# Kernel tuning notes

Measured on AMD Instinct MI355X. Metric: run time of the kernel, lower is better.

Reference implementation:

```python
import jax, jax.numpy as jnp
import numpy as np

B, S, VOCAB, HID, NCLS = 64, 512, 1400, 256, 128


def _time_lstm(W_all, b_all, U_all, b_u, W_d, b_d, x, ts):
    # x: [b, s, h], ts: [b, s]
    b = x.shape[0]
    h0 = jnp.zeros((b, HID), x.dtype)
    c0 = jnp.zeros((b, HID), x.dtype)

    def step(carry, xt):
        h, c = carry
        x_t, t_t = xt  # [b,h], [b]
        c_s1 = jnp.tanh(c @ W_d.T + b_d)
        c_adj = (c - c_s1) + c_s1 * t_t[:, None]
        gates = jax.nn.sigmoid(h @ W_all.T + b_all + x_t @ U_all.T + b_u)
        f, i, o, c_tmp = jnp.split(gates, 4, axis=1)  # note: c_tmp is sigmoid, as in source
        c_new = f * c_adj + i * c_tmp
        h_new = o * jnp.tanh(c_new)
        return (h_new, c_new), h_new

    _, hs = jax.lax.scan(step, (h0, c0), (x.transpose(1, 0, 2), ts.T))
    return hs.transpose(1, 0, 2)  # [b, s, h]


def setup_inputs() -> dict:
    key = jax.random.key(0)
    ks = jax.random.split(key, 18)

    def g(k, shape, scale=0.05):
        return jax.random.normal(k, shape, dtype=jnp.float32) * scale

    return {
        "inputs": jax.random.uniform(ks[0], (B, S, VOCAB), dtype=jnp.float32),
        "timestamps": jax.random.uniform(ks[1], (B, S), dtype=jnp.float32),
        "emb": g(ks[2], (VOCAB, HID)),
        "W_all1": g(ks[3], (4 * HID, HID)), "b_all1": g(ks[4], (4 * HID,)),
        "U_all1": g(ks[5], (4 * HID, HID)), "b_u1": g(ks[6], (4 * HID,)),
        "W_d1": g(ks[7], (HID, HID)), "b_d1": g(ks[8], (HID,)),
        "W_all2": g(ks[9], (4 * HID, HID)), "b_all2": g(ks[10], (4 * HID,)),
        "U_all2": g(ks[11], (4 * HID, HID)), "b_u2": g(ks[12], (4 * HID,)),
        "W_d2": g(ks[13], (HID, HID)), "b_d2": g(ks[14], (HID,)),
        "wa": g(ks[15], (1, HID)),
        "Wb": g(ks[16], (HID, HID)),
        "W_out": g(ks[17], (NCLS, HID)),
    }


def reference(inputs, timestamps, emb, W_all1, b_all1, U_all1, b_u1, W_d1, b_d1,
              W_all2, b_all2, U_all2, b_u2, W_d2, b_d2, wa, Wb, W_out):
    embedded = jnp.einsum('bsv,vh->bsh', inputs, emb)  # multi-hot embedding lookup
    out1 = _time_lstm(W_all1, b_all1, U_all1, b_u1, W_d1, b_d1, embedded, timestamps)
    out2 = _time_lstm(W_all2, b_all2, U_all2, b_u2, W_d2, b_d2, embedded, timestamps)
    alpha = jax.nn.softmax(jnp.einsum('bsh,oh->bs', out1, wa), axis=1)  # [b,s]
    Beta = jnp.tanh(jnp.einsum('bsh,gh->bsg', out2, Wb))  # [b,s,h]
    ctx = jnp.sum(embedded * Beta * alpha[:, :, None], axis=1)  # [b,h]
    return ctx @ W_out.T  # [b, num_classes]
```

## Files before the change

kernel.cpp:

```cpp
#include <hip/hip_runtime.h>

typedef __attribute__((ext_vector_type(8))) short short8;
typedef __attribute__((ext_vector_type(4))) float f32x4;
typedef __attribute__((ext_vector_type(4))) unsigned int u32x4;

#define B_   64
#define S_   512
#define V_   1400
#define VP_  1408
#define H_   256
#define G4_  1024
#define NC_  128
#define CH_  64

__device__ __forceinline__ unsigned short f2bf(float f) {
    unsigned u = __builtin_bit_cast(unsigned, f);
    u += 0x7FFFu + ((u >> 16) & 1u);
    return (unsigned short)(u >> 16);
}
__device__ __forceinline__ float bf2f(unsigned short h) {
    unsigned u = ((unsigned)h) << 16;
    return __builtin_bit_cast(float, u);
}
__device__ __forceinline__ float fsig(float x) {
    x = fminf(fmaxf(x, -40.f), 40.f);
    float e = __builtin_amdgcn_exp2f(x * -1.44269504f);
    return __builtin_amdgcn_rcpf(1.0f + e);
}
__device__ __forceinline__ float ftanh(float x) {
    x = fminf(fmaxf(x, -40.f), 40.f);
    float e = __builtin_amdgcn_exp2f(x * 2.88539008f);
    return 1.0f - 2.0f * __builtin_amdgcn_rcpf(e + 1.0f);
}

__device__ __forceinline__ short8 gload16_sc1(const unsigned short* p) {
    short8 r;
    asm volatile("global_load_dwordx4 %0, %1, off sc1"
                 : "=&v"(r) : "v"((unsigned long long)p));
    return r;
}
__device__ __forceinline__ void gstore_short_sc1(unsigned short* p, unsigned v) {
    asm volatile("global_store_short %0, %1, off sc1"
                 :: "v"((unsigned long long)p), "v"(v));
}
__device__ __forceinline__ short8 gload16_sc0(const unsigned short* p) {
    short8 r;
    asm volatile("global_load_dwordx4 %0, %1, off sc0"
                 : "=&v"(r) : "v"((unsigned long long)p));
    return r;
}
__device__ __forceinline__ void gstore_short_plain(unsigned short* p, unsigned v) {
    asm volatile("global_store_short %0, %1, off"
                 :: "v"((unsigned long long)p), "v"(v));
}
__device__ __forceinline__ void gstore_dword_plain(unsigned int* p, unsigned v) {
    asm volatile("global_store_dword %0, %1, off"
                 :: "v"((unsigned long long)p), "v"(v));
}
__device__ __forceinline__ void gpoll16_plain(const unsigned int* p,
                                              u32x4& f0, u32x4& f1, u32x4& f2, u32x4& f3) {
    asm volatile("global_load_dwordx4 %0, %4, off\n\t"
                 "global_load_dwordx4 %1, %5, off\n\t"
                 "global_load_dwordx4 %2, %6, off\n\t"
                 "global_load_dwordx4 %3, %7, off\n\t"
                 "s_waitcnt vmcnt(0)"
                 : "=&v"(f0), "=&v"(f1), "=&v"(f2), "=&v"(f3)
                 : "v"((unsigned long long)p),        "v"((unsigned long long)(p + 4)),
                   "v"((unsigned long long)(p + 8)),  "v"((unsigned long long)(p + 12)));
}

#define CNT_ZONE_ 38912

__global__ void k0_prep(const float* __restrict__ emb,
                        const float* __restrict__ Wa1, const float* __restrict__ Wa2,
                        const float* __restrict__ Wd1, const float* __restrict__ Wd2,
                        const float* __restrict__ U1,  const float* __restrict__ U2,
                        const float* __restrict__ ba1, const float* __restrict__ bu1,
                        const float* __restrict__ ba2, const float* __restrict__ bu2,
                        const float* __restrict__ Wb,
                        unsigned short* __restrict__ embT, unsigned short* __restrict__ Wg,
                        unsigned short* __restrict__ Wd,   unsigned short* __restrict__ Ub,
                        unsigned short* __restrict__ Wbb,  float* __restrict__ bg,
                        unsigned int* __restrict__ cnt) {
    int tid = blockIdx.x * blockDim.x + threadIdx.x;
    int np = gridDim.x * blockDim.x;
    for (int i = tid; i < 256 * VP_; i += np) {
        int n = i / VP_, k = i - n * VP_;
        embT[i] = (k < V_) ? f2bf(emb[k * H_ + n]) : (unsigned short)0;
    }
    for (int i = tid; i < G4_ * H_; i += np) {
        Wg[i] = f2bf(Wa1[i]); Wg[G4_ * H_ + i] = f2bf(Wa2[i]);
        Ub[i] = f2bf(U1[i]);  Ub[G4_ * H_ + i] = f2bf(U2[i]);
    }
    for (int i = tid; i < H_ * H_; i += np) {
        Wd[i] = f2bf(Wd1[i]); Wd[H_ * H_ + i] = f2bf(Wd2[i]); Wbb[i] = f2bf(Wb[i]);
    }
    for (int i = tid; i < G4_; i += np) {
        bg[i] = ba1[i] + bu1[i]; bg[G4_ + i] = ba2[i] + bu2[i];
    }
    for (int i = tid; i < CNT_ZONE_; i += np) cnt[i] = 0;
}

__global__ __launch_bounds__(512, 2) void k1_embed(const float* __restrict__ inputs,
                                                   const unsigned short* __restrict__ embT,
                                                   unsigned short* __restrict__ embB) {
    const int tid = threadIdx.x;
    const int w = tid >> 6, ln = tid & 63, q = ln >> 4, l16 = ln & 15;
    const int mt = w >> 2, ng = (w & 3) * 4;
    const int Rbase = blockIdx.x * 32 + mt * 16;
    const float* arow = inputs + (long)(Rbase + l16) * V_;

    f32x4 acc[4];
    #pragma unroll
    for (int i = 0; i < 4; ++i) acc[i] = (f32x4){0.f, 0.f, 0.f, 0.f};

    for (int kt = 0; kt < 44; ++kt) {
        int k0 = kt * 32 + q * 8;
        short8 af;
        if (kt == 43 && q == 3) {
            #pragma unroll
            for (int j = 0; j < 8; ++j) af[j] = 0;
        } else {
            f32x4 x0 = *(const f32x4*)(arow + k0);
            f32x4 x1 = *(const f32x4*)(arow + k0 + 4);
            #pragma unroll
            for (int j = 0; j < 4; ++j) { af[j] = (short)f2bf(x0[j]); af[4 + j] = (short)f2bf(x1[j]); }
        }
        #pragma unroll
        for (int i = 0; i < 4; ++i) {
            short8 bf = *(const short8*)(embT + (long)((ng + i) * 16 + l16) * VP_ + k0);
            acc[i] = __builtin_amdgcn_mfma_f32_16x16x32_bf16(af, bf, acc[i], 0, 0, 0);
        }
    }
    #pragma unroll
    for (int i = 0; i < 4; ++i) {
        int col = (ng + i) * 16 + l16;
        #pragma unroll
        for (int j = 0; j < 4; ++j) {
            int R = Rbase + 4 * q + j;
            embB[(long)R * H_ + col] = f2bf(acc[i][j]);
        }
    }
}

__global__ __launch_bounds__(512, 2) void k2_pre(const unsigned short* __restrict__ embB,
                                                 const unsigned short* __restrict__ Ub,
                                                 const float* __restrict__ bg,
                                                 float* __restrict__ P, int t0) {
    const int tid = threadIdx.x;
    const int w = tid >> 6, ln = tid & 63, q = ln >> 4, l16 = ln & 15;
    const int rbase = blockIdx.x * 32;

    short8 af[2][8];
    #pragma unroll
    for (int mt = 0; mt < 2; ++mt)
        #pragma unroll
        for (int kt = 0; kt < 8; ++kt) {
            int rp = rbase + mt * 16 + l16;
            int rg = t0 * 64 + rp;
            int b = rg & 63, s = rg >> 6;
            af[mt][kt] = *(const short8*)(embB + ((long)b * S_ + s) * H_ + kt * 32 + q * 8);
        }

    for (int i = 0; i < 16; ++i) {
        int nt2 = w * 16 + i;
        int l = nt2 >> 6;
        int gcol = (nt2 & 63) * 16 + l16;
        float bias = bg[nt2 * 16 + l16];
        short8 bf[8];
        #pragma unroll
        for (int kt = 0; kt < 8; ++kt)
            bf[kt] = *(const short8*)(Ub + (long)(nt2 * 16 + l16) * H_ + kt * 32 + q * 8);
        #pragma unroll
        for (int mt = 0; mt < 2; ++mt) {
            f32x4 acc = (f32x4){bias, bias, bias, bias};
            #pragma unroll
            for (int kt = 0; kt < 8; ++kt)
                acc = __builtin_amdgcn_mfma_f32_16x16x32_bf16(af[mt][kt], bf[kt], acc, 0, 0, 0);
            int rp0 = rbase + mt * 16;
            float* dst = P + ((long)l * (CH_ * 64) + rp0 + 4 * q) * G4_ + gcol;
            #pragma unroll
            for (int j = 0; j < 4; ++j) dst[(long)j * G4_] = acc[j];
        }
    }
}

__global__ __launch_bounds__(256, 1) void k3_fused(const float* __restrict__ ts,
                                                   const unsigned short* __restrict__ W,
                                                   const float* __restrict__ bd1,
                                                   const float* __restrict__ bd2,
                                                   const float* __restrict__ Pcur,
                                                   unsigned short* __restrict__ out1,
                                                   unsigned short* __restrict__ out2,
                                                   float* __restrict__ cst,
                                                   unsigned short* __restrict__ cx,
                                                   unsigned int* __restrict__ cnt,
                                                   int t0,
                                                   const unsigned short* __restrict__ embB,
                                                   const unsigned short* __restrict__ Ub,
                                                   const float* __restrict__ bg,
                                                   float* __restrict__ Pnext,
                                                   int next_t0) {
    const int tid = threadIdx.x;
    const int w = tid >> 6, ln = tid & 63, q = ln >> 4, l16 = ln & 15;
    const int bid = blockIdx.x;

    if (bid >= 32) {
        const int g2 = bid - 32;
        const int rbase = (g2 >> 1) * 32;
        const int hb = g2 & 1;

        short8 af[2][8];
        #pragma unroll
        for (int mt = 0; mt < 2; ++mt)
            #pragma unroll
            for (int kt = 0; kt < 8; ++kt) {
                int rp = rbase + mt * 16 + l16;
                int rg = next_t0 * 64 + rp;
                int b = rg & 63, s = rg >> 6;
                af[mt][kt] = *(const short8*)(embB + ((long)b * S_ + s) * H_ + kt * 32 + q * 8);
            }

        for (int i = 0; i < 16; ++i) {
            int nt2 = hb * 64 + w * 16 + i;
            int l = nt2 >> 6;
            int gcol = (nt2 & 63) * 16 + l16;
            float bias = bg[nt2 * 16 + l16];
            short8 bf[8];
            #pragma unroll
            for (int kt = 0; kt < 8; ++kt)
                bf[kt] = *(const short8*)(Ub + (long)(nt2 * 16 + l16) * H_ + kt * 32 + q * 8);
            #pragma unroll
            for (int mt = 0; mt < 2; ++mt) {
                f32x4 acc = (f32x4){bias, bias, bias, bias};
                #pragma unroll
                for (int kt = 0; kt < 8; ++kt)
                    acc = __builtin_amdgcn_mfma_f32_16x16x32_bf16(af[mt][kt], bf[kt], acc, 0, 0, 0);
                int rp0 = rbase + mt * 16;
                float* dst = Pnext + ((long)l * (CH_ * 64) + rp0 + 4 * q) * G4_ + gcol;
                #pragma unroll
                for (int j = 0; j < 4; ++j) dst[(long)j * G4_] = acc[j];
            }
        }
        return;
    }

    __shared__ float ts_lds[16][CH_];
    const int chunk = t0 >> 6;

    const int myx = (int)__builtin_amdgcn_s_getreg(63508);
    unsigned int* rdy  = cnt + 4096 + chunk * 64;
    int*          xpub = (int*)(cnt + 4608);
    if (tid == 0) {
        __hip_atomic_store(&xpub[bid], myx, __ATOMIC_RELAXED, __HIP_MEMORY_SCOPE_AGENT);
        __hip_atomic_fetch_add(rdy, 1u, __ATOMIC_RELEASE, __HIP_MEMORY_SCOPE_AGENT);
    }
    unsigned hs_it = 0;
    while (__hip_atomic_load(rdy, __ATOMIC_ACQUIRE, __HIP_MEMORY_SCOPE_AGENT) < 32u
           && ++hs_it < (1u << 20))
        __builtin_amdgcn_s_sleep(2);
    int xv[32];
    #pragma unroll
    for (int i = 0; i < 32; ++i)
        xv[i] = __hip_atomic_load(&xpub[i], __ATOMIC_RELAXED, __HIP_MEMORY_SCOPE_AGENT);
    unsigned okA = 1, inr = 1, mask = 0;
    #pragma unroll
    for (int g = 0; g < 8; ++g)
        okA &= (unsigned)((xv[g] == xv[g + 8]) & (xv[g] == xv[g + 16]) & (xv[g] == xv[g + 24]));
    #pragma unroll
    for (int i = 0; i < 32; ++i) {
        inr &= (unsigned)((unsigned)xv[i] < 8u);
        mask |= 1u << ((unsigned)xv[i] & 31u);
    }
    const bool fast = okA && inr && (mask == 0xFFu) && (hs_it < (1u << 20));

    const int grp = bid & 7, cg = bid >> 3;
    const int l = grp >> 2, m = grp & 3, b0 = m * 16;
    const int hc0 = cg * 64 + w * 16;
    const int mycol = hc0 + l16;
    unsigned int* cell = cnt + (chunk * 8 + grp) * 64;
    unsigned int* fbase = cnt + 6144 + (long)chunk * 64 * 64;
    unsigned short* outp = l ? out2 : out1;
    const float bdv = (l ? bd2 : bd1)[mycol];

    for (int i = tid; i < 16 * CH_; i += 256) {
        int r = i >> 6, cc = i & (CH_ - 1);
        ts_lds[r][cc] = ts[(b0 + r) * S_ + t0 + cc];
    }

    short8 wg[4][8];
    short8 wd[8];
    #pragma unroll
    for (int g = 0; g < 4; ++g)
        #pragma unroll
        for (int kt = 0; kt < 8; ++kt)
            wg[g][kt] = *(const short8*)(W + ((long)(l * G4_ + g * H_ + mycol)) * H_ + kt * 32 + q * 8);
    #pragma unroll
    for (int kt = 0; kt < 8; ++kt)
        wd[kt] = *(const short8*)(W + (long)2 * G4_ * H_ + ((long)(l * H_ + mycol)) * H_ + kt * 32 + q * 8);

    float cf[4];
    if (t0 == 0) {
        cf[0] = cf[1] = cf[2] = cf[3] = 0.f;
    } else {
        #pragma unroll
        for (int j = 0; j < 4; ++j)
            cf[j] = cst[(long)(l * 4 + m) * 4096 + (4 * q + j) * 256 + mycol];
    }
    __syncthreads();

    const float* Pbase = Pcur + ((long)l * (CH_ * 64) + b0) * G4_;

    if (fast) {
        unsigned opaque_zero;
        asm volatile("v_mov_b32 %0, 0" : "=v"(opaque_zero));

        float pv[4][4];
        #pragma unroll
        for (int g = 0; g < 4; ++g)
            #pragma unroll
            for (int j = 0; j < 4; ++j)
                pv[g][j] = Pbase[((long)(4 * q + j)) * G4_ + g * H_ + mycol];
        asm volatile("" ::: "memory");

        #pragma unroll 1
        for (int t = 0; t < CH_; ++t) {
            const int gt = t0 + t;

            if (t) {
                const unsigned int* fprev = fbase + (long)(t - 1) * 64;
                u32x4 f0, f1, f2, f3;
                gpoll16_plain(fprev, f0, f1, f2, f3);
                unsigned s = 0;
                #pragma unroll
                for (int i = 0; i < 4; ++i) s += f0[i] + f1[i] + f2[i] + f3[i];
                if (s != 16u) {
                    const unsigned tgt = 16u * (unsigned)t;
                    unsigned it = 0;
                    for (;;) {
                        unsigned v = 0;
                        if (ln == 0)
                            v = __hip_atomic_fetch_add(cell, opaque_zero,
                                                       __ATOMIC_RELAXED, __HIP_MEMORY_SCOPE_WORKGROUP);
                        v = __shfl(v, 0);
                        if (v >= tgt || ++it >= (1u << 14)) break;
                    }
                }
            }
            __builtin_amdgcn_fence(__ATOMIC_ACQUIRE, "agent");
            __builtin_amdgcn_sched_barrier(0);

            short8 ha[8], ca[8];
            if (gt == 0) {
                #pragma unroll
                for (int kt = 0; kt < 8; ++kt) {
                    #pragma unroll
                    for (int j = 0; j < 8; ++j) { ha[kt][j] = 0; ca[kt][j] = 0; }
                }
            } else {
                const unsigned short* crow = cx + ((long)(((gt - 1) & 1) * 8 + grp)) * 4096 + l16 * 256 + q * 8;
                const unsigned short* hrow = outp + ((long)(b0 + l16) * S_ + (gt - 1)) * H_ + q * 8;
                #pragma unroll
                for (int kt = 0; kt < 8; ++kt) ca[kt] = gload16_sc0(crow + kt * 32);
                #pragma unroll
                for (int kt = 0; kt < 8; ++kt) ha[kt] = gload16_sc0(hrow + kt * 32);
            }
            asm volatile("s_waitcnt vmcnt(8)" ::: "memory");
            __builtin_amdgcn_sched_barrier(0);

            f32x4 dacc = (f32x4){bdv, bdv, bdv, bdv};
            #pragma unroll
            for (int kt = 0; kt < 8; ++kt)
                dacc = __builtin_amdgcn_mfma_f32_16x16x32_bf16(ca[kt], wd[kt], dacc, 0, 0, 0);

            asm volatile("s_waitcnt vmcnt(0)" ::: "memory");
            __builtin_amdgcn_sched_barrier(0);

            f32x4 gacc[4];
            #pragma unroll
            for (int g = 0; g < 4; ++g) {
                gacc[g] = (f32x4){pv[g][0], pv[g][1], pv[g][2], pv[g][3]};
                #pragma unroll
                for (int kt = 0; kt < 8; ++kt)
                    gacc[g] = __builtin_amdgcn_mfma_f32_16x16x32_bf16(ha[kt], wg[g][kt], gacc[g], 0, 0, 0);
            }

            #pragma unroll
            for (int j = 0; j < 4; ++j) {
                int r = 4 * q + j;
                float tv = ts_lds[r][t];
                float cs1 = ftanh(dacc[j]);
                float cadj = cf[j] + cs1 * (tv - 1.0f);
                float fg = fsig(gacc[0][j]), ig = fsig(gacc[1][j]);
                float og = fsig(gacc[2][j]), ct = fsig(gacc[3][j]);
                float cn = fg * cadj + ig * ct;
                float hn = og * ftanh(cn);
                cf[j] = cn;
                gstore_short_plain(outp + ((long)(b0 + r) * S_ + gt) * H_ + mycol, (unsigned)f2bf(hn));
                gstore_short_plain(cx + ((long)((gt & 1) * 8 + grp)) * 4096 + r * 256 + mycol, (unsigned)f2bf(cn));
            }
            asm volatile("s_waitcnt vmcnt(0)" ::: "memory");
            if (ln == 0) {
                gstore_dword_plain(fbase + (long)t * 64 + (cg * 4 + w), 1u);
                (void)__hip_atomic_fetch_add(cell, 1u, __ATOMIC_RELAXED, __HIP_MEMORY_SCOPE_WORKGROUP);
            }

            {
                int tn = (t + 1 < CH_) ? t + 1 : t;
                asm volatile("" ::: "memory");
                #pragma unroll
                for (int g = 0; g < 4; ++g)
                    #pragma unroll
                    for (int j = 0; j < 4; ++j)
                        pv[g][j] = Pbase[((long)tn * 64 + 4 * q + j) * G4_ + g * H_ + mycol];
                asm volatile("" ::: "memory");
            }
        }
    } else {
        #pragma unroll 1
        for (int t = 0; t < CH_; ++t) {
            const int gt = t0 + t;

            float pv[4][4];
            #pragma unroll
            for (int g = 0; g < 4; ++g)
                #pragma unroll
                for (int j = 0; j < 4; ++j)
                    pv[g][j] = Pbase[((long)t * 64 + 4 * q + j) * G4_ + g * H_ + mycol];
            asm volatile("" ::: "memory");

            {
                unsigned tgt = 4u * (unsigned)t, it = 0;
                while (__hip_atomic_load(cell, __ATOMIC_RELAXED, __HIP_MEMORY_SCOPE_AGENT) < tgt
                       && ++it < (1u << 18))
                    __builtin_amdgcn_s_sleep(1);
            }

            short8 ha[8], ca[8];
            if (gt == 0) {
                #pragma unroll
                for (int kt = 0; kt < 8; ++kt) {
                    #pragma unroll
                    for (int j = 0; j < 8; ++j) { ha[kt][j] = 0; ca[kt][j] = 0; }
                }
            } else {
                const unsigned short* crow = cx + ((long)(((gt - 1) & 1) * 8 + grp)) * 4096 + l16 * 256 + q * 8;
                const unsigned short* hrow = outp + ((long)(b0 + l16) * S_ + (gt - 1)) * H_ + q * 8;
                #pragma unroll
                for (int kt = 0; kt < 8; ++kt) ca[kt] = gload16_sc1(crow + kt * 32);
                #pragma unroll
                for (int kt = 0; kt < 8; ++kt) ha[kt] = gload16_sc1(hrow + kt * 32);
            }
            asm volatile("s_waitcnt vmcnt(8)" ::: "memory");
            __builtin_amdgcn_sched_barrier(0);

            f32x4 dacc = (f32x4){bdv, bdv, bdv, bdv};
            #pragma unroll
            for (int kt = 0; kt < 8; ++kt)
                dacc = __builtin_amdgcn_mfma_f32_16x16x32_bf16(ca[kt], wd[kt], dacc, 0, 0, 0);

            asm volatile("s_waitcnt vmcnt(0)" ::: "memory");
            __builtin_amdgcn_sched_barrier(0);

            f32x4 gacc[4];
            #pragma unroll
            for (int g = 0; g < 4; ++g) {
                gacc[g] = (f32x4){pv[g][0], pv[g][1], pv[g][2], pv[g][3]};
                #pragma unroll
                for (int kt = 0; kt < 8; ++kt)
                    gacc[g] = __builtin_amdgcn_mfma_f32_16x16x32_bf16(ha[kt], wg[g][kt], gacc[g], 0, 0, 0);
            }

            #pragma unroll
            for (int j = 0; j < 4; ++j) {
                int r = 4 * q + j;
                float tv = ts_lds[r][t];
                float cs1 = ftanh(dacc[j]);
                float cadj = cf[j] + cs1 * (tv - 1.0f);
                float fg = fsig(gacc[0][j]), ig = fsig(gacc[1][j]);
                float og = fsig(gacc[2][j]), ct = fsig(gacc[3][j]);
                float cn = fg * cadj + ig * ct;
                float hn = og * ftanh(cn);
                cf[j] = cn;
                gstore_short_sc1(outp + ((long)(b0 + r) * S_ + gt) * H_ + mycol, (unsigned)f2bf(hn));
                gstore_short_sc1(cx + ((long)((gt & 1) * 8 + grp)) * 4096 + r * 256 + mycol, (unsigned)f2bf(cn));
            }
            asm volatile("s_waitcnt vmcnt(0)" ::: "memory");
            __syncthreads();
            if (tid == 0) atomicAdd(cell, 1u);
        }
    }

    #pragma unroll
    for (int j = 0; j < 4; ++j)
        cst[(long)(l * 4 + m) * 4096 + (4 * q + j) * 256 + mycol] = cf[j];
}

__global__ __launch_bounds__(512) void k4a_alpha(const unsigned short* __restrict__ out1,
                                                 const float* __restrict__ wa,
                                                 float* __restrict__ alpha) {
    __shared__ float sc[512];
    __shared__ float red[512];
    const int b = blockIdx.x, tid = threadIdx.x;
    const int w = tid >> 6, ln = tid & 63;
    f32x4 wv = *(const f32x4*)(wa + ln * 4);
    for (int i = 0; i < 64; ++i) {
        int s = w * 64 + i;
        const unsigned short* row = out1 + ((long)b * S_ + s) * H_ + ln * 4;
        float d = bf2f(row[0]) * wv[0] + bf2f(row[1]) * wv[1] +
                  bf2f(row[2]) * wv[2] + bf2f(row[3]) * wv[3];
        #pragma unroll
        for (int off = 32; off; off >>= 1) d += __shfl_xor(d, off);
        if (ln == 0) sc[s] = d;
    }
    __syncthreads();
    float v = sc[tid];
    red[tid] = v;
    for (int st = 256; st; st >>= 1) {
        __syncthreads();
        if (tid < st) red[tid] = fmaxf(red[tid], red[tid + st]);
    }
    __syncthreads();
    float M = red[0];
    __syncthreads();
    float e = __builtin_amdgcn_exp2f((v - M) * 1.44269504f);
    red[tid] = e;
    for (int st = 256; st; st >>= 1) {
        __syncthreads();
        if (tid < st) red[tid] += red[tid + st];
    }
    __syncthreads();
    alpha[b * S_ + tid] = e * __builtin_amdgcn_rcpf(red[0]);
}

__global__ __launch_bounds__(512, 2) void k4b_ctx(const unsigned short* __restrict__ out2,
                                                  const unsigned short* __restrict__ Wbb,
                                                  const unsigned short* __restrict__ embB,
                                                  const float* __restrict__ alpha,
                                                  float* __restrict__ ctx) {
    __shared__ float cbuf[32][256];
    const int b = blockIdx.x, tid = threadIdx.x;
    const int w = tid >> 6, ln = tid & 63, q = ln >> 4, l16 = ln & 15;

    float cp[16];
    #pragma unroll
    for (int nt = 0; nt < 16; ++nt) cp[nt] = 0.f;

    for (int i = 0; i < 4; ++i) {
        int mt = w * 4 + i;
        short8 af[8];
        #pragma unroll
        for (int kt = 0; kt < 8; ++kt)
            af[kt] = *(const short8*)(out2 + ((long)b * S_ + mt * 16 + l16) * H_ + kt * 32 + q * 8);
        float al[4];
        #pragma unroll
        for (int j = 0; j < 4; ++j) al[j] = alpha[b * S_ + mt * 16 + 4 * q + j];
        for (int nt = 0; nt < 16; ++nt) {
            f32x4 acc = (f32x4){0.f, 0.f, 0.f, 0.f};
            #pragma unroll
            for (int kt = 0; kt < 8; ++kt) {
                short8 bf = *(const short8*)(Wbb + (long)(nt * 16 + l16) * H_ + kt * 32 + q * 8);
                acc = __builtin_amdgcn_mfma_f32_16x16x32_bf16(af[kt], bf, acc, 0, 0, 0);
            }
            #pragma unroll
            for (int j = 0; j < 4; ++j) {
                int s = mt * 16 + 4 * q + j;
                float beta = ftanh(acc[j]);
                float ev = bf2f(embB[((long)b * S_ + s) * H_ + nt * 16 + l16]);
                cp[nt] += beta * al[j] * ev;
            }
        }
    }
    #pragma unroll
    for (int nt = 0; nt < 16; ++nt) cbuf[w * 4 + q][nt * 16 + l16] = cp[nt];
    __syncthreads();
    if (tid < 256) {
        float sum = 0.f;
        for (int i = 0; i < 32; ++i) sum += cbuf[i][tid];
        ctx[b * H_ + tid] = sum;
    }
}

__global__ void k4c_out(const float* __restrict__ ctx, const float* __restrict__ Wout,
                        float* __restrict__ out) {
    int b = blockIdx.x, n = threadIdx.x;
    const f32x4* cr = (const f32x4*)(ctx + b * H_);
    const f32x4* wr = (const f32x4*)(Wout + n * H_);
    float acc = 0.f;
    #pragma unroll 8
    for (int i = 0; i < 64; ++i) {
        f32x4 c = cr[i], ww = wr[i];
        acc += c[0] * ww[0] + c[1] * ww[1] + c[2] * ww[2] + c[3] * ww[3];
    }
    out[b * NC_ + n] = acc;
}

extern "C" void kernel_launch(void* const* d_in, const int* in_sizes, int n_in,
                              void* d_out, int out_size, void* d_ws, size_t ws_size,
                              hipStream_t stream) {
    (void)in_sizes; (void)n_in; (void)out_size;
    const float* inputs = (const float*)d_in[0];
    const float* tsp    = (const float*)d_in[1];
    const float* emb    = (const float*)d_in[2];
    const float* Wa1 = (const float*)d_in[3];  const float* ba1 = (const float*)d_in[4];
    const float* U1  = (const float*)d_in[5];  const float* bu1 = (const float*)d_in[6];
    const float* Wd1 = (const float*)d_in[7];  const float* bd1 = (const float*)d_in[8];
    const float* Wa2 = (const float*)d_in[9];  const float* ba2 = (const float*)d_in[10];
    const float* U2  = (const float*)d_in[11]; const float* bu2 = (const float*)d_in[12];
    const float* Wd2 = (const float*)d_in[13]; const float* bd2 = (const float*)d_in[14];
    const float* wa  = (const float*)d_in[15];
    const float* Wb  = (const float*)d_in[16];
    const float* Wout = (const float*)d_in[17];
    float* out = (float*)d_out;

    char* ws = (char*)d_ws;
    unsigned short* embT = (unsigned short*)(ws + 0);
    unsigned short* Wg   = (unsigned short*)(ws + 720896);
    unsigned short* Wd   = (unsigned short*)(ws + 1769472);
    unsigned short* Ub   = (unsigned short*)(ws + 2031616);
    unsigned short* Wbb  = (unsigned short*)(ws + 3080192);
    float*          bgp  = (float*)(ws + 3211264);
    unsigned short* embB = (unsigned short*)(ws + 3219456);
    float*          P0   = (float*)(ws + 19996672);
    unsigned short* out1 = (unsigned short*)(ws + 53551104);
    unsigned short* out2 = (unsigned short*)(ws + 70328320);
    unsigned short* cx   = (unsigned short*)(ws + 87105536);
    float*          cst  = (float*)(ws + 87236608);
    float*          alp  = (float*)(ws + 87367680);
    float*          ctx  = (float*)(ws + 87498752);
    unsigned int*   cnt  = (unsigned int*)(ws + 87564288);
    float*          P1   = (float*)(ws + 87719936);
    const size_t NEED_FUSED = 121274368;
    const bool fuse = (ws_size >= NEED_FUSED);

    hipLaunchKernelGGL(k0_prep, dim3(256), dim3(256), 0, stream,
                       emb, Wa1, Wa2, Wd1, Wd2, U1, U2, ba1, bu1, ba2, bu2, Wb,
                       embT, Wg, Wd, Ub, Wbb, bgp, cnt);
    hipLaunchKernelGGL(k1_embed, dim3(1024), dim3(512), 0, stream, inputs, embT, embB);
    hipLaunchKernelGGL(k2_pre, dim3(128), dim3(512), 0, stream, embB, Ub, bgp, P0, 0);

    float* Pb[2] = { P0, fuse ? P1 : P0 };
    for (int c = 0; c < 8; ++c) {
        if (fuse) {
            int ng = (c < 7) ? 256 : 0;
            hipLaunchKernelGGL(k3_fused, dim3(32 + ng), dim3(256), 0, stream,
                               tsp, Wg, bd1, bd2, Pb[c & 1], out1, out2, cst, cx, cnt, c * CH_,
                               embB, Ub, bgp, Pb[(c + 1) & 1], (c + 1) * CH_);
        } else {
            if (c > 0)
                hipLaunchKernelGGL(k2_pre, dim3(128), dim3(512), 0, stream, embB, Ub, bgp, P0, c * CH_);
            hipLaunchKernelGGL(k3_fused, dim3(32), dim3(256), 0, stream,
                               tsp, Wg, bd1, bd2, P0, out1, out2, cst, cx, cnt, c * CH_,
                               embB, Ub, bgp, P0, S_ );
        }
    }
    hipLaunchKernelGGL(k4a_alpha, dim3(64), dim3(512), 0, stream, out1, wa, alp);
    hipLaunchKernelGGL(k4b_ctx, dim3(64), dim3(512), 0, stream, out2, Wbb, embB, alp, ctx);
    hipLaunchKernelGGL(k4c_out, dim3(64), dim3(128), 0, stream, ctx, Wout, out);
}
```

Measured before the change: 2.822 ms.

## Use per-group monotonic step flags and prefetch next projections before gate MFMAs

Per-timestep one-shot flags are replaced by one reusable flag slot per wave per group that stores a monotonically increasing step count. Consumers now spin on a 16-flag poll with an acquire fence each iteration and only fall back to the atomic counter after many retries. The prefetch of the next step's input projections also moves earlier, ahead of the gate MFMAs, so it overlaps compute rather than the flag publish. The aim is lower inter-block synchronisation latency in the recurrent loop, at the cost of repeated acquire fences in the spin loop and a changed flag memory layout.

```diff
diff --git a/kernel.cpp b/kernel.cpp
--- a/kernel.cpp
+++ b/kernel.cpp
@@ -279,7 +279,7 @@
     const int hc0 = cg * 64 + w * 16;
     const int mycol = hc0 + l16;
     unsigned int* cell = cnt + (chunk * 8 + grp) * 64;
-    unsigned int* fbase = cnt + 6144 + (long)chunk * 64 * 64;
+    unsigned int* fl   = cnt + 6144 + (chunk * 8 + grp) * 64;
     unsigned short* outp = l ? out2 : out1;
     const float bdv = (l ? bd2 : bd1)[mycol];
 
@@ -328,26 +328,36 @@
             const int gt = t0 + t;
 
             if (t) {
-                const unsigned int* fprev = fbase + (long)(t - 1) * 64;
-                u32x4 f0, f1, f2, f3;
-                gpoll16_plain(fprev, f0, f1, f2, f3);
-                unsigned s = 0;
-                #pragma unroll
-                for (int i = 0; i < 4; ++i) s += f0[i] + f1[i] + f2[i] + f3[i];
-                if (s != 16u) {
-                    const unsigned tgt = 16u * (unsigned)t;
-                    unsigned it = 0;
-                    for (;;) {
-                        unsigned v = 0;
-                        if (ln == 0)
-                            v = __hip_atomic_fetch_add(cell, opaque_zero,
-                                                       __ATOMIC_RELAXED, __HIP_MEMORY_SCOPE_WORKGROUP);
-                        v = __shfl(v, 0);
-                        if (v >= tgt || ++it >= (1u << 14)) break;
+                const unsigned tt = (unsigned)t;
+                unsigned it = 0;
+                for (;;) {
+                    __builtin_amdgcn_fence(__ATOMIC_ACQUIRE, "agent");
+                    u32x4 f0, f1, f2, f3;
+                    gpoll16_plain(fl, f0, f1, f2, f3);
+                    unsigned ok = 1;
+                    #pragma unroll
+                    for (int i = 0; i < 4; ++i)
+                        ok &= (unsigned)(f0[i] >= tt) & (unsigned)(f1[i] >= tt) &
+                              (unsigned)(f2[i] >= tt) & (unsigned)(f3[i] >= tt);
+                    if (ok) break;
+                    if (++it >= (1u << 13)) {
+                        const unsigned tgt = 16u * tt;
+                        unsigned it2 = 0;
+                        for (;;) {
+                            unsigned v = 0;
+                            if (ln == 0)
+                                v = __hip_atomic_fetch_add(cell, opaque_zero,
+                                                           __ATOMIC_RELAXED, __HIP_MEMORY_SCOPE_WORKGROUP);
+                            v = __shfl(v, 0);
+                            if (v >= tgt || ++it2 >= (1u << 14)) break;
+                        }
+                        __builtin_amdgcn_fence(__ATOMIC_ACQUIRE, "agent");
+                        break;
                     }
                 }
-            }
-            __builtin_amdgcn_fence(__ATOMIC_ACQUIRE, "agent");
+            } else {
+                __builtin_amdgcn_fence(__ATOMIC_ACQUIRE, "agent");
+            }
             __builtin_amdgcn_sched_barrier(0);
 
             short8 ha[8], ca[8];
@@ -378,8 +388,22 @@
 
             f32x4 gacc[4];
             #pragma unroll
+            for (int g = 0; g < 4; ++g)
+                gacc[g] = (f32x4){pv[g][0], pv[g][1], pv[g][2], pv[g][3]};
+
+            __builtin_amdgcn_sched_barrier(0);
+            {
+                int tn = (t + 1 < CH_) ? t + 1 : t;
+                #pragma unroll
+                for (int g = 0; g < 4; ++g)
+                    #pragma unroll
+                    for (int j = 0; j < 4; ++j)
+                        pv[g][j] = Pbase[((long)tn * 64 + 4 * q + j) * G4_ + g * H_ + mycol];
+            }
+            __builtin_amdgcn_sched_barrier(0);
+
+            #pragma unroll
             for (int g = 0; g < 4; ++g) {
-                gacc[g] = (f32x4){pv[g][0], pv[g][1], pv[g][2], pv[g][3]};
                 #pragma unroll
                 for (int kt = 0; kt < 8; ++kt)
                     gacc[g] = __builtin_amdgcn_mfma_f32_16x16x32_bf16(ha[kt], wg[g][kt], gacc[g], 0, 0, 0);
@@ -401,19 +425,9 @@
             }
             asm volatile("s_waitcnt vmcnt(0)" ::: "memory");
             if (ln == 0) {
-                gstore_dword_plain(fbase + (long)t * 64 + (cg * 4 + w), 1u);
-                (void)__hip_atomic_fetch_add(cell, 1u, __ATOMIC_RELAXED, __HIP_MEMORY_SCOPE_WORKGROUP);
-            }
-
-            {
-                int tn = (t + 1 < CH_) ? t + 1 : t;
-                asm volatile("" ::: "memory");
-                #pragma unroll
-                for (int g = 0; g < 4; ++g)
-                    #pragma unroll
-                    for (int j = 0; j < 4; ++j)
-                        pv[g][j] = Pbase[((long)tn * 64 + 4 * q + j) * G4_ + g * H_ + mycol];
-                asm volatile("" ::: "memory");
+                gstore_dword_plain(fl + (cg * 4 + w), (unsigned)(t + 1));
+                (void)__hip_atomic_fetch_add(cell, 1u, __ATOMIC_RELAXED,
+                                             __HIP_MEMORY_SCOPE_WORKGROUP);
             }
         }
     } else {
```

New measurement: 3.041 ms. 7.7% more time.

## Split recurrent LSTM step across two blocks per group with LDS-local state

Applied to the files above, without the earlier changes.

The recurrent kernel drops from 32 to 16 blocks. Each block now owns half of the hidden columns for a batch group and keeps its own half of h and c in LDS, along with the decay weight slice. Each step reads only the peer half from global memory and syncs with a single peer counter, replacing the 4-way flag polling. The intent is to cut global traffic and cross-block synchronization per timestep, at the cost of more MFMA work and register pressure per block and fewer blocks sharing the load.

```diff
diff --git a/kernel.cpp b/kernel.cpp
--- a/kernel.cpp
+++ b/kernel.cpp
@@ -2,7 +2,6 @@
 
 typedef __attribute__((ext_vector_type(8))) short short8;
 typedef __attribute__((ext_vector_type(4))) float f32x4;
-typedef __attribute__((ext_vector_type(4))) unsigned int u32x4;
 
 #define B_   64
 #define S_   512
@@ -53,23 +52,8 @@
     asm volatile("global_store_short %0, %1, off"
                  :: "v"((unsigned long long)p), "v"(v));
 }
-__device__ __forceinline__ void gstore_dword_plain(unsigned int* p, unsigned v) {
-    asm volatile("global_store_dword %0, %1, off"
-                 :: "v"((unsigned long long)p), "v"(v));
-}
-__device__ __forceinline__ void gpoll16_plain(const unsigned int* p,
-                                              u32x4& f0, u32x4& f1, u32x4& f2, u32x4& f3) {
-    asm volatile("global_load_dwordx4 %0, %4, off\n\t"
-                 "global_load_dwordx4 %1, %5, off\n\t"
-                 "global_load_dwordx4 %2, %6, off\n\t"
-                 "global_load_dwordx4 %3, %7, off\n\t"
-                 "s_waitcnt vmcnt(0)"
-                 : "=&v"(f0), "=&v"(f1), "=&v"(f2), "=&v"(f3)
-                 : "v"((unsigned long long)p),        "v"((unsigned long long)(p + 4)),
-                   "v"((unsigned long long)(p + 8)),  "v"((unsigned long long)(p + 12)));
-}
-
-#define CNT_ZONE_ 38912
+
+#define CNT_ZONE_ 9216
 
 __global__ void k0_prep(const float* __restrict__ emb,
                         const float* __restrict__ Wa1, const float* __restrict__ Wa2,
@@ -205,8 +189,8 @@
     const int w = tid >> 6, ln = tid & 63, q = ln >> 4, l16 = ln & 15;
     const int bid = blockIdx.x;
 
-    if (bid >= 32) {
-        const int g2 = bid - 32;
+    if (bid >= 16) {
+        const int g2 = bid - 16;
         const int rbase = (g2 >> 1) * 32;
         const int hb = g2 & 1;
 
@@ -246,254 +230,251 @@
     }
 
     __shared__ float ts_lds[16][CH_];
+    __shared__ unsigned short h_loc[16][136];
+    __shared__ unsigned short c_loc[16][136];
+    __shared__ unsigned short wd_lds[128][264];
     const int chunk = t0 >> 6;
 
     const int myx = (int)__builtin_amdgcn_s_getreg(63508);
-    unsigned int* rdy  = cnt + 4096 + chunk * 64;
-    int*          xpub = (int*)(cnt + 4608);
+    unsigned int* rdy  = cnt + 8192 + chunk * 64;
+    int*          xpub = (int*)(cnt + 8704);
     if (tid == 0) {
         __hip_atomic_store(&xpub[bid], myx, __ATOMIC_RELAXED, __HIP_MEMORY_SCOPE_AGENT);
         __hip_atomic_fetch_add(rdy, 1u, __ATOMIC_RELEASE, __HIP_MEMORY_SCOPE_AGENT);
     }
     unsigned hs_it = 0;
-    while (__hip_atomic_load(rdy, __ATOMIC_ACQUIRE, __HIP_MEMORY_SCOPE_AGENT) < 32u
+    while (__hip_atomic_load(rdy, __ATOMIC_ACQUIRE, __HIP_MEMORY_SCOPE_AGENT) < 16u
            && ++hs_it < (1u << 20))
         __builtin_amdgcn_s_sleep(2);
-    int xv[32];
-    #pragma unroll
-    for (int i = 0; i < 32; ++i)
+    int xv[16];
+    #pragma unroll
+    for (int i = 0; i < 16; ++i)
         xv[i] = __hip_atomic_load(&xpub[i], __ATOMIC_RELAXED, __HIP_MEMORY_SCOPE_AGENT);
-    unsigned okA = 1, inr = 1, mask = 0;
+    unsigned okP = 1, inr = 1, mask = 0;
     #pragma unroll
     for (int g = 0; g < 8; ++g)
-        okA &= (unsigned)((xv[g] == xv[g + 8]) & (xv[g] == xv[g + 16]) & (xv[g] == xv[g + 24]));
-    #pragma unroll
-    for (int i = 0; i < 32; ++i) {
+        okP &= (unsigned)(xv[g] == xv[g + 8]);
+    #pragma unroll
+    for (int i = 0; i < 16; ++i) {
         inr &= (unsigned)((unsigned)xv[i] < 8u);
         mask |= 1u << ((unsigned)xv[i] & 31u);
     }
-    const bool fast = okA && inr && (mask == 0xFFu) && (hs_it < (1u << 20));
-
-    const int grp = bid & 7, cg = bid >> 3;
+    const bool fast = okP && inr && (mask == 0xFFu) && (hs_it < (1u << 20));
+
+    const int grp = bid & 7, half = bid >> 3;
     const int l = grp >> 2, m = grp & 3, b0 = m * 16;
-    const int hc0 = cg * 64 + w * 16;
-    const int mycol = hc0 + l16;
-    unsigned int* cell = cnt + (chunk * 8 + grp) * 64;
-    unsigned int* fbase = cnt + 6144 + (long)chunk * 64 * 64;
+    const int colB0 = w * 32;
+    unsigned int* own_cell  = cnt + (((chunk * 8 + grp) * 2) + half) * 64;
+    unsigned int* peer_cell = cnt + (((chunk * 8 + grp) * 2) + (half ^ 1)) * 64;
     unsigned short* outp = l ? out2 : out1;
-    const float bdv = (l ? bd2 : bd1)[mycol];
+    const float* bdp = l ? bd2 : bd1;
+    float bdv[2];
+    bdv[0] = bdp[half * 128 + colB0 + l16];
+    bdv[1] = bdp[half * 128 + colB0 + 16 + l16];
 
     for (int i = tid; i < 16 * CH_; i += 256) {
         int r = i >> 6, cc = i & (CH_ - 1);
         ts_lds[r][cc] = ts[(b0 + r) * S_ + t0 + cc];
     }
-
-    short8 wg[4][8];
-    short8 wd[8];
+    for (int i = tid; i < 128 * 2; i += 256) {
+        int ri = i >> 1, k0 = (i & 1) * 128;
+        const unsigned short* src = W + (long)2 * G4_ * H_ + ((long)(l * H_ + half * 128 + ri)) * H_ + k0;
+        #pragma unroll
+        for (int c8 = 0; c8 < 128; c8 += 8)
+            *(short8*)&wd_lds[ri][k0 + c8] = *(const short8*)(src + c8);
+    }
+
+    short8 wg[4][2][8];
     #pragma unroll
     for (int g = 0; g < 4; ++g)
         #pragma unroll
-        for (int kt = 0; kt < 8; ++kt)
-            wg[g][kt] = *(const short8*)(W + ((long)(l * G4_ + g * H_ + mycol)) * H_ + kt * 32 + q * 8);
-    #pragma unroll
-    for (int kt = 0; kt < 8; ++kt)
-        wd[kt] = *(const short8*)(W + (long)2 * G4_ * H_ + ((long)(l * H_ + mycol)) * H_ + kt * 32 + q * 8);
-
-    float cf[4];
+        for (int ct = 0; ct < 2; ++ct)
+            #pragma unroll
+            for (int kt = 0; kt < 8; ++kt)
+                wg[g][ct][kt] = *(const short8*)(W +
+                    ((long)(l * G4_ + g * H_ + half * 128 + colB0 + ct * 16 + l16)) * H_ + kt * 32 + q * 8);
+
+    float cf[2][4];
     if (t0 == 0) {
-        cf[0] = cf[1] = cf[2] = cf[3] = 0.f;
+        #pragma unroll
+        for (int ct = 0; ct < 2; ++ct)
+            #pragma unroll
+            for (int j = 0; j < 4; ++j) cf[ct][j] = 0.f;
+        for (int i = tid; i < 16 * 16; i += 256) {
+            int r = i >> 4, c8 = (i & 15) * 8;
+            short8 z;
+            #pragma unroll
+            for (int jj = 0; jj < 8; ++jj) z[jj] = 0;
+            *(short8*)&h_loc[r][c8] = z;
+            *(short8*)&c_loc[r][c8] = z;
+        }
     } else {
         #pragma unroll
-        for (int j = 0; j < 4; ++j)
-            cf[j] = cst[(long)(l * 4 + m) * 4096 + (4 * q + j) * 256 + mycol];
+        for (int ct = 0; ct < 2; ++ct)
+            #pragma unroll
+            for (int j = 0; j < 4; ++j)
+                cf[ct][j] = cst[(long)(l * 4 + m) * 4096 + (4 * q + j) * 256 + half * 128 + colB0 + ct * 16 + l16];
+        for (int i = tid; i < 16 * 16; i += 256) {
+            int r = i >> 4, c8 = (i & 15) * 8;
+            *(short8*)&h_loc[r][c8] =
+                *(const short8*)(outp + ((long)(b0 + r) * S_ + (t0 - 1)) * H_ + half * 128 + c8);
+            const float* cp = cst + (long)(l * 4 + m) * 4096 + r * 256 + half * 128 + c8;
+            short8 cv;
+            #pragma unroll
+            for (int jj = 0; jj < 8; ++jj) cv[jj] = (short)f2bf(cp[jj]);
+            *(short8*)&c_loc[r][c8] = cv;
+        }
     }
     __syncthreads();
 
     const float* Pbase = Pcur + ((long)l * (CH_ * 64) + b0) * G4_;
-
-    if (fast) {
-        unsigned opaque_zero;
-        asm volatile("v_mov_b32 %0, 0" : "=v"(opaque_zero));
-
-        float pv[4][4];
+    unsigned opaque_zero;
+    asm volatile("v_mov_b32 %0, 0" : "=v"(opaque_zero));
+
+    #pragma unroll 1
+    for (int t = 0; t < CH_; ++t) {
+        const int gt = t0 + t;
+
+        if (t > 0) {
+            const unsigned tgt = 4u * (unsigned)t;
+            unsigned it = 0;
+            for (;;) {
+                unsigned v = 0;
+                if (ln == 0)
+                    v = __hip_atomic_fetch_add(peer_cell, opaque_zero,
+                                               __ATOMIC_RELAXED, __HIP_MEMORY_SCOPE_AGENT);
+                v = __shfl(v, 0);
+                if (v >= tgt || ++it >= (1u << 14)) break;
+            }
+            if (fast) __builtin_amdgcn_fence(__ATOMIC_ACQUIRE, "agent");
+        }
+        __builtin_amdgcn_sched_barrier(0);
+
+        short8 har[4], car[4];
+        if (gt == 0) {
+            #pragma unroll
+            for (int kt2 = 0; kt2 < 4; ++kt2) {
+                #pragma unroll
+                for (int jj = 0; jj < 8; ++jj) { har[kt2][jj] = 0; car[kt2][jj] = 0; }
+            }
+        } else {
+            const unsigned short* crow = cx + ((long)(((gt - 1) & 1) * 8 + grp)) * 4096
+                                           + l16 * 256 + (half ^ 1) * 128 + q * 8;
+            const unsigned short* hrow = outp + ((long)(b0 + l16) * S_ + (gt - 1)) * H_
+                                              + (half ^ 1) * 128 + q * 8;
+            if (fast) {
+                #pragma unroll
+                for (int kt2 = 0; kt2 < 4; ++kt2) car[kt2] = gload16_sc0(crow + kt2 * 32);
+                #pragma unroll
+                for (int kt2 = 0; kt2 < 4; ++kt2) har[kt2] = gload16_sc0(hrow + kt2 * 32);
+            } else {
+                #pragma unroll
+                for (int kt2 = 0; kt2 < 4; ++kt2) car[kt2] = gload16_sc1(crow + kt2 * 32);
+                #pragma unroll
+                for (int kt2 = 0; kt2 < 4; ++kt2) har[kt2] = gload16_sc1(hrow + kt2 * 32);
+            }
+        }
+        float pv[4][2][4];
         #pragma unroll
         for (int g = 0; g < 4; ++g)
             #pragma unroll
-            for (int j = 0; j < 4; ++j)
-                pv[g][j] = Pbase[((long)(4 * q + j)) * G4_ + g * H_ + mycol];
-        asm volatile("" ::: "memory");
-
-        #pragma unroll 1
-        for (int t = 0; t < CH_; ++t) {
-            const int gt = t0 + t;
-
-            if (t) {
-                const unsigned int* fprev = fbase + (long)(t - 1) * 64;
-                u32x4 f0, f1, f2, f3;
-                gpoll16_plain(fprev, f0, f1, f2, f3);
-                unsigned s = 0;
-                #pragma unroll
-                for (int i = 0; i < 4; ++i) s += f0[i] + f1[i] + f2[i] + f3[i];
-                if (s != 16u) {
-                    const unsigned tgt = 16u * (unsigned)t;
-                    unsigned it = 0;
-                    for (;;) {
-                        unsigned v = 0;
-                        if (ln == 0)
-                            v = __hip_atomic_fetch_add(cell, opaque_zero,
-                                                       __ATOMIC_RELAXED, __HIP_MEMORY_SCOPE_WORKGROUP);
-                        v = __shfl(v, 0);
-                        if (v >= tgt || ++it >= (1u << 14)) break;
-                    }
+            for (int ct = 0; ct < 2; ++ct)
+                #pragma unroll
+                for (int j = 0; j < 4; ++j)
+                    pv[g][ct][j] = Pbase[((long)t * 64 + 4 * q + j) * G4_
+                                         + g * H_ + half * 128 + colB0 + ct * 16 + l16];
+
+        f32x4 dacc[2];
+        dacc[0] = (f32x4){bdv[0], bdv[0], bdv[0], bdv[0]};
+        dacc[1] = (f32x4){bdv[1], bdv[1], bdv[1], bdv[1]};
+        f32x4 gacc[4][2];
+        #pragma unroll
+        for (int g = 0; g < 4; ++g)
+            #pragma unroll
+            for (int ct = 0; ct < 2; ++ct) gacc[g][ct] = (f32x4){0.f, 0.f, 0.f, 0.f};
+
+        if (gt > 0) {
+            #pragma unroll
+            for (int kt2 = 0; kt2 < 4; ++kt2) {
+                const int ktg = half * 4 + kt2;
+                short8 cl = *(const short8*)&c_loc[l16][kt2 * 32 + q * 8];
+                #pragma unroll
+                for (int ct = 0; ct < 2; ++ct) {
+                    short8 wdf = *(const short8*)&wd_lds[colB0 + ct * 16 + l16][ktg * 32 + q * 8];
+                    dacc[ct] = __builtin_amdgcn_mfma_f32_16x16x32_bf16(cl, wdf, dacc[ct], 0, 0, 0);
                 }
-            }
-            __builtin_amdgcn_fence(__ATOMIC_ACQUIRE, "agent");
-            __builtin_amdgcn_sched_barrier(0);
-
-            short8 ha[8], ca[8];
-            if (gt == 0) {
-                #pragma unroll
-                for (int kt = 0; kt < 8; ++kt) {
+                short8 hl = *(const short8*)&h_loc[l16][kt2 * 32 + q * 8];
+                #pragma unroll
+                for (int g = 0; g < 4; ++g)
                     #pragma unroll
-                    for (int j = 0; j < 8; ++j) { ha[kt][j] = 0; ca[kt][j] = 0; }
+                    for (int ct = 0; ct < 2; ++ct)
+                        gacc[g][ct] = __builtin_amdgcn_mfma_f32_16x16x32_bf16(hl, wg[g][ct][ktg], gacc[g][ct], 0, 0, 0);
+            }
+        }
+
+        asm volatile("s_waitcnt vmcnt(0)" ::: "memory");
+        __builtin_amdgcn_sched_barrier(0);
+        if (gt > 0) {
+            #pragma unroll
+            for (int kt2 = 0; kt2 < 4; ++kt2) {
+                const int ktg = (half ^ 1) * 4 + kt2;
+                #pragma unroll
+                for (int ct = 0; ct < 2; ++ct) {
+                    short8 wdf = *(const short8*)&wd_lds[colB0 + ct * 16 + l16][ktg * 32 + q * 8];
+                    dacc[ct] = __builtin_amdgcn_mfma_f32_16x16x32_bf16(car[kt2], wdf, dacc[ct], 0, 0, 0);
                 }
-            } else {
-                const unsigned short* crow = cx + ((long)(((gt - 1) & 1) * 8 + grp)) * 4096 + l16 * 256 + q * 8;
-                const unsigned short* hrow = outp + ((long)(b0 + l16) * S_ + (gt - 1)) * H_ + q * 8;
-                #pragma unroll
-                for (int kt = 0; kt < 8; ++kt) ca[kt] = gload16_sc0(crow + kt * 32);
-                #pragma unroll
-                for (int kt = 0; kt < 8; ++kt) ha[kt] = gload16_sc0(hrow + kt * 32);
-            }
-            asm volatile("s_waitcnt vmcnt(8)" ::: "memory");
-            __builtin_amdgcn_sched_barrier(0);
-
-            f32x4 dacc = (f32x4){bdv, bdv, bdv, bdv};
-            #pragma unroll
-            for (int kt = 0; kt < 8; ++kt)
-                dacc = __builtin_amdgcn_mfma_f32_16x16x32_bf16(ca[kt], wd[kt], dacc, 0, 0, 0);
-
-            asm volatile("s_waitcnt vmcnt(0)" ::: "memory");
-            __builtin_amdgcn_sched_barrier(0);
-
-            f32x4 gacc[4];
-            #pragma unroll
-            for (int g = 0; g < 4; ++g) {
-                gacc[g] = (f32x4){pv[g][0], pv[g][1], pv[g][2], pv[g][3]};
-                #pragma unroll
-                for (int kt = 0; kt < 8; ++kt)
-                    gacc[g] = __builtin_amdgcn_mfma_f32_16x16x32_bf16(ha[kt], wg[g][kt], gacc[g], 0, 0, 0);
-            }
-
+                #pragma unroll
+                for (int g = 0; g < 4; ++g)
+                    #pragma unroll
+                    for (int ct = 0; ct < 2; ++ct)
+                        gacc[g][ct] = __builtin_amdgcn_mfma_f32_16x16x32_bf16(har[kt2], wg[g][ct][ktg], gacc[g][ct], 0, 0, 0);
+            }
+        }
+
+        __syncthreads();
+
+        #pragma unroll
+        for (int ct = 0; ct < 2; ++ct) {
             #pragma unroll
             for (int j = 0; j < 4; ++j) {
                 int r = 4 * q + j;
                 float tv = ts_lds[r][t];
-                float cs1 = ftanh(dacc[j]);
-                float cadj = cf[j] + cs1 * (tv - 1.0f);
-                float fg = fsig(gacc[0][j]), ig = fsig(gacc[1][j]);
-                float og = fsig(gacc[2][j]), ct = fsig(gacc[3][j]);
-                float cn = fg * cadj + ig * ct;
+                float cs1 = ftanh(dacc[ct][j]);
+                float cadj = cf[ct][j] + cs1 * (tv - 1.0f);
+                float fg = fsig(gacc[0][ct][j] + pv[0][ct][j]);
+                float ig = fsig(gacc[1][ct][j] + pv[1][ct][j]);
+                float og = fsig(gacc[2][ct][j] + pv[2][ct][j]);
+                float cg = fsig(gacc[3][ct][j] + pv[3][ct][j]);
+                float cn = fg * cadj + ig * cg;
                 float hn = og * ftanh(cn);
-                cf[j] = cn;
-                gstore_short_plain(outp + ((long)(b0 + r) * S_ + gt) * H_ + mycol, (unsigned)f2bf(hn));
-                gstore_short_plain(cx + ((long)((gt & 1) * 8 + grp)) * 4096 + r * 256 + mycol, (unsigned)f2bf(cn));
-            }
-            asm volatile("s_waitcnt vmcnt(0)" ::: "memory");
-            if (ln == 0) {
-                gstore_dword_plain(fbase + (long)t * 64 + (cg * 4 + w), 1u);
-                (void)__hip_atomic_fetch_add(cell, 1u, __ATOMIC_RELAXED, __HIP_MEMORY_SCOPE_WORKGROUP);
-            }
-
-            {
-                int tn = (t + 1 < CH_) ? t + 1 : t;
-                asm volatile("" ::: "memory");
-                #pragma unroll
-                for (int g = 0; g < 4; ++g)
-                    #pragma unroll
-                    for (int j = 0; j < 4; ++j)
-                        pv[g][j] = Pbase[((long)tn * 64 + 4 * q + j) * G4_ + g * H_ + mycol];
-                asm volatile("" ::: "memory");
-            }
-        }
-    } else {
-        #pragma unroll 1
-        for (int t = 0; t < CH_; ++t) {
-            const int gt = t0 + t;
-
-            float pv[4][4];
-            #pragma unroll
-            for (int g = 0; g < 4; ++g)
-                #pragma unroll
-                for (int j = 0; j < 4; ++j)
-                    pv[g][j] = Pbase[((long)t * 64 + 4 * q + j) * G4_ + g * H_ + mycol];
-            asm volatile("" ::: "memory");
-
-            {
-                unsigned tgt = 4u * (unsigned)t, it = 0;
-                while (__hip_atomic_load(cell, __ATOMIC_RELAXED, __HIP_MEMORY_SCOPE_AGENT) < tgt
-                       && ++it < (1u << 18))
-                    __builtin_amdgcn_s_sleep(1);
-            }
-
-            short8 ha[8], ca[8];
-            if (gt == 0) {
-                #pragma unroll
-                for (int kt = 0; kt < 8; ++kt) {
-                    #pragma unroll
-                    for (int j = 0; j < 8; ++j) { ha[kt][j] = 0; ca[kt][j] = 0; }
+                cf[ct][j] = cn;
+                unsigned short hb = f2bf(hn), cb = f2bf(cn);
+                int colB = colB0 + ct * 16 + l16;
+                h_loc[r][colB] = hb;
+                c_loc[r][colB] = cb;
+                int mycol = half * 128 + colB;
+                if (fast) {
+                    gstore_short_plain(outp + ((long)(b0 + r) * S_ + gt) * H_ + mycol, (unsigned)hb);
+                    gstore_short_plain(cx + ((long)((gt & 1) * 8 + grp)) * 4096 + r * 256 + mycol, (unsigned)cb);
+                } else {
+                    gstore_short_sc1(outp + ((long)(b0 + r) * S_ + gt) * H_ + mycol, (unsigned)hb);
+                    gstore_short_sc1(cx + ((long)((gt & 1) * 8 + grp)) * 4096 + r * 256 + mycol, (unsigned)cb);
                 }
-            } else {
-                const unsigned short* crow = cx + ((long)(((gt - 1) & 1) * 8 + grp)) * 4096 + l16 * 256 + q * 8;
-                const unsigned short* hrow = outp + ((long)(b0 + l16) * S_ + (gt - 1)) * H_ + q * 8;
-                #pragma unroll
-                for (int kt = 0; kt < 8; ++kt) ca[kt] = gload16_sc1(crow + kt * 32);
-                #pragma unroll
-                for (int kt = 0; kt < 8; ++kt) ha[kt] = gload16_sc1(hrow + kt * 32);
-            }
-            asm volatile("s_waitcnt vmcnt(8)" ::: "memory");
-            __builtin_amdgcn_sched_barrier(0);
-
-            f32x4 dacc = (f32x4){bdv, bdv, bdv, bdv};
-            #pragma unroll
-            for (int kt = 0; kt < 8; ++kt)
-                dacc = __builtin_amdgcn_mfma_f32_16x16x32_bf16(ca[kt], wd[kt], dacc, 0, 0, 0);
-
-            asm volatile("s_waitcnt vmcnt(0)" ::: "memory");
-            __builtin_amdgcn_sched_barrier(0);
-
-            f32x4 gacc[4];
-            #pragma unroll
-            for (int g = 0; g < 4; ++g) {
-                gacc[g] = (f32x4){pv[g][0], pv[g][1], pv[g][2], pv[g][3]};
-                #pragma unroll
-                for (int kt = 0; kt < 8; ++kt)
-                    gacc[g] = __builtin_amdgcn_mfma_f32_16x16x32_bf16(ha[kt], wg[g][kt], gacc[g], 0, 0, 0);
-            }
-
-            #pragma unroll
-            for (int j = 0; j < 4; ++j) {
-                int r = 4 * q + j;
-                float tv = ts_lds[r][t];
-                float cs1 = ftanh(dacc[j]);
-                float cadj = cf[j] + cs1 * (tv - 1.0f);
-                float fg = fsig(gacc[0][j]), ig = fsig(gacc[1][j]);
-                float og = fsig(gacc[2][j]), ct = fsig(gacc[3][j]);
-                float cn = fg * cadj + ig * ct;
-                float hn = og * ftanh(cn);
-                cf[j] = cn;
-                gstore_short_sc1(outp + ((long)(b0 + r) * S_ + gt) * H_ + mycol, (unsigned)f2bf(hn));
-                gstore_short_sc1(cx + ((long)((gt & 1) * 8 + grp)) * 4096 + r * 256 + mycol, (unsigned)f2bf(cn));
-            }
-            asm volatile("s_waitcnt vmcnt(0)" ::: "memory");
-            __syncthreads();
-            if (tid == 0) atomicAdd(cell, 1u);
-        }
-    }
-
-    #pragma unroll
-    for (int j = 0; j < 4; ++j)
-        cst[(long)(l * 4 + m) * 4096 + (4 * q + j) * 256 + mycol] = cf[j];
+            }
+        }
+
+        asm volatile("s_waitcnt vmcnt(0)" ::: "memory");
+        if (ln == 0)
+            (void)__hip_atomic_fetch_add(own_cell, 1u, __ATOMIC_RELAXED, __HIP_MEMORY_SCOPE_AGENT);
+
+        __syncthreads();
+    }
+
+    #pragma unroll
+    for (int ct = 0; ct < 2; ++ct)
+        #pragma unroll
+        for (int j = 0; j < 4; ++j)
+            cst[(long)(l * 4 + m) * 4096 + (4 * q + j) * 256 + half * 128 + colB0 + ct * 16 + l16] = cf[ct][j];
 }
 
 __global__ __launch_bounds__(512) void k4a_alpha(const unsigned short* __restrict__ out1,
@@ -643,13 +624,13 @@
     for (int c = 0; c < 8; ++c) {
         if (fuse) {
             int ng = (c < 7) ? 256 : 0;
-            hipLaunchKernelGGL(k3_fused, dim3(32 + ng), dim3(256), 0, stream,
+            hipLaunchKernelGGL(k3_fused, dim3(16 + ng), dim3(256), 0, stream,
                                tsp, Wg, bd1, bd2, Pb[c & 1], out1, out2, cst, cx, cnt, c * CH_,
                                embB, Ub, bgp, Pb[(c + 1) & 1], (c + 1) * CH_);
         } else {
             if (c > 0)
                 hipLaunchKernelGGL(k2_pre, dim3(128), dim3(512), 0, stream, embB, Ub, bgp, P0, c * CH_);
-            hipLaunchKernelGGL(k3_fused, dim3(32), dim3(256), 0, stream,
+            hipLaunchKernelGGL(k3_fused, dim3(16), dim3(256), 0, stream,
                                tsp, Wg, bd1, bd2, P0, out1, out2, cst, cx, cnt, c * CH_,
                                embB, Ub, bgp, P0, S_ );
         }
```

Result: slower. 6.815 ms (+141.5%).
